# Kernel tuning notes

Hardware: AMD Instinct MI355X
Metric: run time of the kernel (lower is better)

Reference implementation:

```python
import jax, jax.numpy as jnp
import numpy as np

IN_CH, IN_DIM, OUT_CH, OUT_DIM = 16, 32, 32, 32
NUM_ITERS = 3
EPS = 1e-11


def setup_inputs() -> dict:
    key = jax.random.key(0)
    kx, kw = jax.random.split(key)
    B, N = 32, 128
    x = jax.random.normal(kx, (B, N, IN_CH, IN_DIM), dtype=jnp.float32)
    # learned transform, matches torch Parameter randn(1,1,in_ch,out_ch,in_dim,out_dim)
    W = jax.random.normal(kw, (IN_CH, OUT_CH, IN_DIM, OUT_DIM), dtype=jnp.float32)
    return {"x": x, "W": W, "number_of_nodes": N}


def squash(s):
    # s: [B, 1, out_ch, out_dim]; squash along capsule dim (axis=3)
    mag_sq = jnp.sum(s * s, axis=3, keepdims=True)
    mag = jnp.sqrt(mag_sq) + EPS
    a_j = mag_sq / (1.0 + mag_sq)
    return a_j * (s / mag), a_j


def reference(x, W, number_of_nodes):
    B, N = x.shape[0], x.shape[1]
    # u_hat[b,n,c,o,j] = sum_i x[b,n,c,i] * W[c,o,i,j]
    u_hat = jnp.einsum('bnci,coij->bncoj', x, W)
    u_hat = u_hat.reshape(B, N * IN_CH, OUT_CH, OUT_DIM)

    b_ij = jnp.zeros((B, N * IN_CH, OUT_CH, 1), dtype=u_hat.dtype)
    v_j = a_j = None
    for _ in range(NUM_ITERS):
        c_ij = jax.nn.softmax(b_ij, axis=1)          # softmax over input capsules
        s_j = jnp.sum(c_ij * u_hat, axis=1, keepdims=True)  # [B,1,out_ch,out_dim]
        v_j, a_j = squash(s_j)
        # agreement: broadcast v_j over input-capsule dim (no explicit cat)
        u_vj = jnp.sum(u_hat * v_j, axis=3, keepdims=True)
        b_ij = b_ij + u_vj
    return v_j, a_j
```

## Files before the change

### kernel.cpp

```cpp
#include <hip/hip_runtime.h>
#include <math.h>

#define BB 32
#define NN 128
#define CC 16
#define OO 32
#define II 32
#define JJ 32
#define MM (NN*CC)
static constexpr float EPS_ = 1e-11f;


__global__ __launch_bounds__(1024) void k_transpose(
    const float* __restrict__ x, float* __restrict__ xT,
    float* __restrict__ x4T) {
  int b = blockIdx.x >> 4, c = blockIdx.x & 15;
  __shared__ __align__(16) float xsT[II][NN + 4];
  int tid = threadIdx.x;
  {
    int n = tid >> 3, i4 = (tid & 7) * 4;
    float4 v = *(const float4*)(x + (((size_t)(b * NN + n)) * CC + c) * II + i4);
    xsT[i4 + 0][n] = v.x; xsT[i4 + 1][n] = v.y;
    xsT[i4 + 2][n] = v.z; xsT[i4 + 3][n] = v.w;
  }
  __syncthreads();
  {
    int i = tid >> 5, n4 = tid & 31;
    float4 v = *(const float4*)(&xsT[i][n4 * 4]);
    ((float4*)(xT + ((size_t)(b * CC + c)) * II * NN))[tid] = v;
  }
  {
    int nf4 = tid >> 5, i = tid & 31;
    float4 v = make_float4(xsT[i][nf4 * 4 + 0], xsT[i][nf4 * 4 + 1],
                           xsT[i][nf4 * 4 + 2], xsT[i][nf4 * 4 + 3]);
    ((float4*)(x4T + ((size_t)(b * CC + c)) * II * NN))[tid] = v;
  }
}

__global__ __launch_bounds__(1024, 4) void k_route(
    const float* __restrict__ xT, const float* __restrict__ x4T,
    const float* __restrict__ W, float* __restrict__ out) {
  int bid = blockIdx.x;
  int b = bid & 31, o0 = (bid >> 5) * 2;
  int tid = threadIdx.x;

  __shared__ __align__(16) float bijL[2][CC][NN];
  __shared__ __align__(16) float coef[2][CC][NN];
  __shared__ float cxs[2][CC][II];
  __shared__ float wv [2][CC][II];
  __shared__ float partA[2][CC][JJ];
  __shared__ float vs[2][JJ];
  __shared__ float redM[CC][2];
  __shared__ float smx[2], srin[2];

  {
    int o = tid >> 9, c = (tid >> 5) & 15, n4 = tid & 31;
    *(float4*)(&bijL[o][c][n4 * 4]) = make_float4(0.f, 0.f, 0.f, 0.f);
  }

  const float4* xTb  = (const float4*)(xT  + (size_t)b * CC * II * NN);
  const float4* x4Tb = (const float4*)(x4T + (size_t)b * CC * II * NN);

  for (int it = 0; it < 3; ++it) {
    {
      int o = tid >> 9, c = (tid >> 5) & 15, n4 = tid & 31;
      float4 cf;
      if (it == 0) {
        float u = 1.0f / (float)MM;
        cf = make_float4(u, u, u, u);
      } else {
        float4 bb = *(const float4*)(&bijL[o][c][n4 * 4]);
        float m = smx[o], r = srin[o];
        cf.x = __expf(bb.x - m) * r; cf.y = __expf(bb.y - m) * r;
        cf.z = __expf(bb.z - m) * r; cf.w = __expf(bb.w - m) * r;
      }
      *(float4*)(&coef[o][c][n4 * 4]) = cf;
    }
    __syncthreads();

    {
      int c = tid >> 6, l = tid & 63, i = l & 31, nh = l >> 5;
      const float4* xr = x4Tb + c * (II * NN / 4) + l;
      float a0 = 0.f, a1 = 0.f;
      #pragma unroll 4
      for (int q = 0; q < 16; ++q) {
        float4 xv = xr[q * 64];
        int nf = 2 * q + nh;
        float4 f0 = *(const float4*)(&coef[0][c][nf * 4]);
        float4 f1 = *(const float4*)(&coef[1][c][nf * 4]);
        a0 += xv.x * f0.x + xv.y * f0.y + xv.z * f0.z + xv.w * f0.w;
        a1 += xv.x * f1.x + xv.y * f1.y + xv.z * f1.z + xv.w * f1.w;
      }
      a0 += __shfl_xor(a0, 32);
      a1 += __shfl_xor(a1, 32);
      if (nh == 0) cxs[0][c][i] = a0;
      else         cxs[1][c][i] = a1;
    }
    __syncthreads();

    {
      int o = tid >> 9, c = (tid >> 5) & 15, j = tid & 31;
      const float* Wp = W + (((size_t)(c * OO + o0 + o)) * II) * JJ + j;
      float acc = 0.f;
      #pragma unroll 8
      for (int i = 0; i < II; ++i)
        acc += cxs[o][c][i] * Wp[i * JJ];
      partA[o][c][j] = acc;
    }
    __syncthreads();

    if (tid < 64) {
      int o = tid >> 5, j = tid & 31;
      float s = 0.f;
      #pragma unroll
      for (int c = 0; c < CC; ++c) s += partA[o][c][j];
      float msq = s * s;
      #pragma unroll
      for (int off = 16; off > 0; off >>= 1) msq += __shfl_xor(msq, off);
      float mag = sqrtf(msq) + EPS_;
      float a   = msq / (1.0f + msq);
      float vv  = a * s / mag;
      if (it == 2) {
        int row = b * OO + (o0 + o);
        out[(size_t)row * JJ + j] = vv;
        if (j == 0) out[BB * OO * JJ + row] = a;
      } else {
        vs[o][j] = vv;
      }
    }
    if (it == 2) break;
    __syncthreads();

    {
      int o = tid >> 9, c = (tid >> 5) & 15, i = tid & 31;
      const float4* Wr = (const float4*)(W + (((size_t)(c * OO + o0 + o)) * II + i) * JJ);
      float acc = 0.f;
      #pragma unroll 4
      for (int q = 0; q < 8; ++q) {
        float4 w4 = Wr[q];
        acc += w4.x * vs[o][q*4+0] + w4.y * vs[o][q*4+1]
             + w4.z * vs[o][q*4+2] + w4.w * vs[o][q*4+3];
      }
      wv[o][c][i] = acc;
    }
    __syncthreads();

    {
      int c = tid >> 6, n4 = (tid >> 1) & 31, s = tid & 1;
      float4 ac0 = make_float4(0.f,0.f,0.f,0.f);
      float4 ac1 = make_float4(0.f,0.f,0.f,0.f);
      #pragma unroll 4
      for (int q = 0; q < 16; ++q) {
        int i = s * 16 + q;
        float4 xv = xTb[c * (II * NN / 4) + i * (NN / 4) + n4];
        float w0 = wv[0][c][i], w1 = wv[1][c][i];
        ac0.x += xv.x * w0; ac0.y += xv.y * w0; ac0.z += xv.z * w0; ac0.w += xv.w * w0;
        ac1.x += xv.x * w1; ac1.y += xv.y * w1; ac1.z += xv.z * w1; ac1.w += xv.w * w1;
      }
      ac0.x += __shfl_xor(ac0.x, 1); ac0.y += __shfl_xor(ac0.y, 1);
      ac0.z += __shfl_xor(ac0.z, 1); ac0.w += __shfl_xor(ac0.w, 1);
      ac1.x += __shfl_xor(ac1.x, 1); ac1.y += __shfl_xor(ac1.y, 1);
      ac1.z += __shfl_xor(ac1.z, 1); ac1.w += __shfl_xor(ac1.w, 1);
      float4 r = (s == 0) ? ac0 : ac1;
      float4 bb = *(const float4*)(&bijL[s][c][n4 * 4]);
      r.x += bb.x; r.y += bb.y; r.z += bb.z; r.w += bb.w;
      *(float4*)(&bijL[s][c][n4 * 4]) = r;

      float m4 = fmaxf(fmaxf(r.x, r.y), fmaxf(r.z, r.w));
      #pragma unroll
      for (int off = 2; off <= 32; off <<= 1)
        m4 = fmaxf(m4, __shfl_xor(m4, off));
      if ((tid & 63) <= 1) redM[c][s] = m4;
      __syncthreads();
      if (tid < 2) {
        float m = redM[0][tid];
        #pragma unroll
        for (int w2 = 1; w2 < CC; ++w2) m = fmaxf(m, redM[w2][tid]);
        smx[tid] = m;
      }
      __syncthreads();
      float mo = smx[s];
      float e = __expf(r.x - mo) + __expf(r.y - mo)
              + __expf(r.z - mo) + __expf(r.w - mo);
      #pragma unroll
      for (int off = 2; off <= 32; off <<= 1) e += __shfl_xor(e, off);
      if ((tid & 63) <= 1) redM[c][s] = e;
      __syncthreads();
      if (tid < 2) {
        float ss = 0.f;
        #pragma unroll
        for (int w2 = 0; w2 < CC; ++w2) ss += redM[w2][tid];
        srin[tid] = 1.0f / ss;
      }
    }
    __syncthreads();
  }
}

extern "C" void kernel_launch(void* const* d_in, const int* in_sizes, int n_in,
                              void* d_out, int out_size, void* d_ws, size_t ws_size,
                              hipStream_t stream) {
  const float* x = (const float*)d_in[0];
  const float* W = (const float*)d_in[1];
  (void)in_sizes; (void)n_in;
  float* out = (float*)d_out; (void)out_size;

  float* xT  = (float*)d_ws;
  float* x4T = xT + (size_t)BB * CC * II * NN;
  (void)ws_size;

  k_transpose<<<BB * CC, 1024, 0, stream>>>(x, xT, x4T);
  k_route<<<BB * (OO / 2), 1024, 0, stream>>>(xT, x4T, W, out);
}
```

Baseline: 127.1 us.

## Cache W slices in registers and fuse softmax coefficients into routing update

Each thread now loads its W column and W row into registers once, before the routing loop, and reuses them for all three iterations instead of re-reading global memory every time. The softmax reduction is restructured so that every thread reads the per-wave max and sum partials directly, which removes two single-thread serial reductions. The normalized coefficients are written straight from the values already in registers, which drops the separate coefficient pass and one barrier per iteration. The cost is about 64 extra VGPRs per thread under a 1024-thread launch bound, so register pressure or spilling is a risk.

```diff
diff --git a/kernel.cpp b/kernel.cpp
--- a/kernel.cpp
+++ b/kernel.cpp
@@ -50,34 +50,35 @@
   __shared__ float wv [2][CC][II];
   __shared__ float partA[2][CC][JJ];
   __shared__ float vs[2][JJ];
-  __shared__ float redM[CC][2];
-  __shared__ float smx[2], srin[2];
+  __shared__ float redM[CC][2], redE[CC][2];
 
   {
     int o = tid >> 9, c = (tid >> 5) & 15, n4 = tid & 31;
     *(float4*)(&bijL[o][c][n4 * 4]) = make_float4(0.f, 0.f, 0.f, 0.f);
+    float u = 1.0f / (float)MM;
+    *(float4*)(&coef[o][c][n4 * 4]) = make_float4(u, u, u, u);
+  }
+
+  float wA[II];
+  {
+    int o = tid >> 9, c = (tid >> 5) & 15, j = tid & 31;
+    const float* Wp = W + (((size_t)(c * OO + o0 + o)) * II) * JJ + j;
+    #pragma unroll
+    for (int i = 0; i < II; ++i) wA[i] = Wp[i * JJ];
+  }
+  float4 wW[8];
+  {
+    int o = tid >> 9, c = (tid >> 5) & 15, i = tid & 31;
+    const float4* Wr = (const float4*)(W + (((size_t)(c * OO + o0 + o)) * II + i) * JJ);
+    #pragma unroll
+    for (int q = 0; q < 8; ++q) wW[q] = Wr[q];
   }
 
   const float4* xTb  = (const float4*)(xT  + (size_t)b * CC * II * NN);
   const float4* x4Tb = (const float4*)(x4T + (size_t)b * CC * II * NN);
+  __syncthreads();
 
   for (int it = 0; it < 3; ++it) {
-    {
-      int o = tid >> 9, c = (tid >> 5) & 15, n4 = tid & 31;
-      float4 cf;
-      if (it == 0) {
-        float u = 1.0f / (float)MM;
-        cf = make_float4(u, u, u, u);
-      } else {
-        float4 bb = *(const float4*)(&bijL[o][c][n4 * 4]);
-        float m = smx[o], r = srin[o];
-        cf.x = __expf(bb.x - m) * r; cf.y = __expf(bb.y - m) * r;
-        cf.z = __expf(bb.z - m) * r; cf.w = __expf(bb.w - m) * r;
-      }
-      *(float4*)(&coef[o][c][n4 * 4]) = cf;
-    }
-    __syncthreads();
-
     {
       int c = tid >> 6, l = tid & 63, i = l & 31, nh = l >> 5;
       const float4* xr = x4Tb + c * (II * NN / 4) + l;
@@ -100,11 +101,10 @@
 
     {
       int o = tid >> 9, c = (tid >> 5) & 15, j = tid & 31;
-      const float* Wp = W + (((size_t)(c * OO + o0 + o)) * II) * JJ + j;
       float acc = 0.f;
-      #pragma unroll 8
+      #pragma unroll
       for (int i = 0; i < II; ++i)
-        acc += cxs[o][c][i] * Wp[i * JJ];
+        acc += cxs[o][c][i] * wA[i];
       partA[o][c][j] = acc;
     }
     __syncthreads();
@@ -133,13 +133,11 @@
 
     {
       int o = tid >> 9, c = (tid >> 5) & 15, i = tid & 31;
-      const float4* Wr = (const float4*)(W + (((size_t)(c * OO + o0 + o)) * II + i) * JJ);
       float acc = 0.f;
-      #pragma unroll 4
+      #pragma unroll
       for (int q = 0; q < 8; ++q) {
-        float4 w4 = Wr[q];
-        acc += w4.x * vs[o][q*4+0] + w4.y * vs[o][q*4+1]
-             + w4.z * vs[o][q*4+2] + w4.w * vs[o][q*4+3];
+        acc += wW[q].x * vs[o][q*4+0] + wW[q].y * vs[o][q*4+1]
+             + wW[q].z * vs[o][q*4+2] + wW[q].w * vs[o][q*4+3];
       }
       wv[o][c][i] = acc;
     }
@@ -168,30 +166,26 @@
 
       float m4 = fmaxf(fmaxf(r.x, r.y), fmaxf(r.z, r.w));
       #pragma unroll
-      for (int off = 2; off <= 32; off <<= 1)
-        m4 = fmaxf(m4, __shfl_xor(m4, off));
-      if ((tid & 63) <= 1) redM[c][s] = m4;
+      for (int off = 2; off <= 32; off <<= 1) m4 = fmaxf(m4, __shfl_xor(m4, off));
+      int wave = tid >> 6;
+      if ((tid & 63) <= 1) redM[wave][s] = m4;
       __syncthreads();
-      if (tid < 2) {
-        float m = redM[0][tid];
-        #pragma unroll
-        for (int w2 = 1; w2 < CC; ++w2) m = fmaxf(m, redM[w2][tid]);
-        smx[tid] = m;
-      }
+      float mo = redM[0][s];
+      #pragma unroll
+      for (int w2 = 1; w2 < CC; ++w2) mo = fmaxf(mo, redM[w2][s]);
+      float ex = __expf(r.x - mo), ey = __expf(r.y - mo),
+            ez = __expf(r.z - mo), ew = __expf(r.w - mo);
+      float e = ex + ey + ez + ew;
+      #pragma unroll
+      for (int off = 2; off <= 32; off <<= 1) e += __shfl_xor(e, off);
+      if ((tid & 63) <= 1) redE[wave][s] = e;
       __syncthreads();
-      float mo = smx[s];
-      float e = __expf(r.x - mo) + __expf(r.y - mo)
-              + __expf(r.z - mo) + __expf(r.w - mo);
-      #pragma unroll
-      for (int off = 2; off <= 32; off <<= 1) e += __shfl_xor(e, off);
-      if ((tid & 63) <= 1) redM[c][s] = e;
-      __syncthreads();
-      if (tid < 2) {
-        float ss = 0.f;
-        #pragma unroll
-        for (int w2 = 0; w2 < CC; ++w2) ss += redM[w2][tid];
-        srin[tid] = 1.0f / ss;
-      }
+      float ss = redE[0][s];
+      #pragma unroll
+      for (int w2 = 1; w2 < CC; ++w2) ss += redE[w2][s];
+      float rin = 1.0f / ss;
+      *(float4*)(&coef[s][c][n4 * 4]) =
+          make_float4(ex * rin, ey * rin, ez * rin, ew * rin);
     }
     __syncthreads();
   }
```

Result: faster. 122.9 us (-3.3%).
